# Optimization experiments

Hardware: AMD Instinct MI355X
Metric: run time of the kernel (lower is better)

## Reference

```python
import jax, jax.numpy as jnp
import numpy as np

B, T, H = 8, 8192, 512
E, R = 4, 16
SCALE = 0.04  # ~1/sqrt(H), keeps activations/logits in a sane range


def setup_inputs() -> dict:
    key = jax.random.key(0)
    ks = jax.random.split(key, 7)
    return {
        "x": jax.random.normal(ks[0], (B, T, H), jnp.float32),
        "gate_w": jax.random.normal(ks[1], (E, H), jnp.float32) * SCALE,
        "thr_w": jax.random.normal(ks[2], (1, H), jnp.float32) * SCALE,
        "fc1_w": jax.random.normal(ks[3], (E, H, H), jnp.float32) * SCALE,
        "lora_A": jax.random.normal(ks[4], (E, H, R), jnp.float32) * SCALE,
        "lora_B": jax.random.normal(ks[5], (E, R, H), jnp.float32) * SCALE,
        "fc2_w": jax.random.normal(ks[6], (E, H, H), jnp.float32) * SCALE,
    }


def reference(x, gate_w, thr_w, fc1_w, lora_A, lora_B, fc2_w):
    b, t, h = x.shape
    e = gate_w.shape[0]
    xf = x.reshape(-1, h)  # [N, H], N = B*T

    # Threshold-gated routing
    gate_logits = jax.nn.softmax(xf @ gate_w.T, axis=-1)          # [N, E]
    thresholds = jax.nn.sigmoid(xf @ thr_w.T) * (1.0 / e)         # [N, 1]
    adapted = gate_logits - thresholds                            # [N, E]
    selected = (adapted >= 0).astype(xf.dtype)                    # [N, E]
    weights = adapted * selected
    wsum = jnp.sum(weights, axis=-1, keepdims=True)
    wsum = jnp.where(wsum == 0, jnp.ones_like(wsum), wsum)
    weights = weights / wsum                                      # [N, E]

    # Experts: fc2(relu(fc1(x)) @ A @ B). Dense over all experts; the
    # weighted combine with zero weights matches the gather/scatter path.
    hidden = jax.nn.relu(jnp.einsum('ni,ehi->neh', xf, fc1_w))    # [N, E, H]
    lo = jnp.einsum('neh,ehr->ner', hidden, lora_A)               # [N, E, R]
    lo = jnp.einsum('ner,ero->neo', lo, lora_B)                   # [N, E, H]
    expert_out = jnp.einsum('neo,edo->ned', lo, fc2_w)            # [N, E, H]

    out = jnp.einsum('ne,ned->nd', weights, expert_out)           # [N, H]
    return out.reshape(b, t, h)
```

## Files before the change

### kernel.cpp

```cpp
#include <hip/hip_runtime.h>
#include <stdint.h>

#define NTOK 65536
#define HD   512
#define EXP  4
#define RK   16

typedef __attribute__((ext_vector_type(8)))  short short8;
typedef __attribute__((ext_vector_type(4)))  float f32x4;
typedef __attribute__((ext_vector_type(16))) float f32x16;

__device__ __forceinline__ unsigned short f2bf(float f) {
  union { float f; unsigned int u; } c; c.f = f;
  return (unsigned short)((c.u + 0x7fffu + ((c.u >> 16) & 1u)) >> 16);
}

__device__ __forceinline__ void gl_lds16(const void* g, void* l) {
  __builtin_amdgcn_global_load_lds((const __attribute__((address_space(1))) void*)g,
                                   (__attribute__((address_space(3))) void*)l, 16, 0, 0);
}

__global__ void convgate(const float* __restrict__ x, const float* __restrict__ gw,
                         const float* __restrict__ tw, unsigned short* __restrict__ xbo,
                         float* __restrict__ gates) {
  const int tid = threadIdx.x;
  const int wave = tid >> 6, lane = tid & 63;
  const int half = lane >> 5, l32 = lane & 31;
  const int base = blockIdx.x * 32 + wave * 8;

  float4 wv[5][4];
#pragma unroll
  for (int e = 0; e < 4; e++) {
    const float4* wr = (const float4*)(gw + e * HD);
#pragma unroll
    for (int j = 0; j < 4; j++) wv[e][j] = wr[l32 * 4 + j];
  }
  {
    const float4* wr = (const float4*)tw;
#pragma unroll
    for (int j = 0; j < 4; j++) wv[4][j] = wr[l32 * 4 + j];
  }

#pragma unroll
  for (int it = 0; it < 4; it++) {
    const int n = base + it * 2 + half;
    const float4* xr = (const float4*)(x + (size_t)n * HD);
    float4 xv[4];
#pragma unroll
    for (int j = 0; j < 4; j++) xv[j] = xr[l32 * 4 + j];

    union { short8 v; unsigned short s[8]; } pa, pb;
    pa.s[0] = f2bf(xv[0].x); pa.s[1] = f2bf(xv[0].y); pa.s[2] = f2bf(xv[0].z); pa.s[3] = f2bf(xv[0].w);
    pa.s[4] = f2bf(xv[1].x); pa.s[5] = f2bf(xv[1].y); pa.s[6] = f2bf(xv[1].z); pa.s[7] = f2bf(xv[1].w);
    pb.s[0] = f2bf(xv[2].x); pb.s[1] = f2bf(xv[2].y); pb.s[2] = f2bf(xv[2].z); pb.s[3] = f2bf(xv[2].w);
    pb.s[4] = f2bf(xv[3].x); pb.s[5] = f2bf(xv[3].y); pb.s[6] = f2bf(xv[3].z); pb.s[7] = f2bf(xv[3].w);
    short8* xo = (short8*)(xbo + (size_t)n * HD + l32 * 16);
    xo[0] = pa.v; xo[1] = pb.v;

    float s[5];
#pragma unroll
    for (int e = 0; e < 5; e++) {
      s[e] = 0.f;
#pragma unroll
      for (int j = 0; j < 4; j++)
        s[e] += xv[j].x * wv[e][j].x + xv[j].y * wv[e][j].y
              + xv[j].z * wv[e][j].z + xv[j].w * wv[e][j].w;
    }
#pragma unroll
    for (int off = 16; off > 0; off >>= 1)
#pragma unroll
      for (int i = 0; i < 5; i++) s[i] += __shfl_xor(s[i], off, 64);

    float m = fmaxf(fmaxf(s[0], s[1]), fmaxf(s[2], s[3]));
    float e0 = expf(s[0] - m), e1 = expf(s[1] - m), e2 = expf(s[2] - m), e3 = expf(s[3] - m);
    float inv = 1.f / (e0 + e1 + e2 + e3);
    float thr = 0.25f / (1.f + expf(-s[4]));
    float a0 = e0 * inv - thr, a1 = e1 * inv - thr, a2 = e2 * inv - thr, a3 = e3 * inv - thr;
    float w0 = a0 > 0.f ? a0 : 0.f, w1 = a1 > 0.f ? a1 : 0.f;
    float w2 = a2 > 0.f ? a2 : 0.f, w3 = a3 > 0.f ? a3 : 0.f;
    float wsum = w0 + w1 + w2 + w3;
    wsum = (wsum == 0.f) ? 1.f : wsum;
    if (l32 < 4) {
      float wval = l32 == 0 ? w0 : l32 == 1 ? w1 : l32 == 2 ? w2 : w3;
      gates[(size_t)n * 4 + l32] = wval / wsum;
    }
  }
}

__global__ void prep_all(const float* __restrict__ fc1w, unsigned short* __restrict__ w1b,
                         const float* __restrict__ la, unsigned short* __restrict__ laT,
                         const float* __restrict__ loraB, const float* __restrict__ fc2,
                         unsigned short* __restrict__ Mt) {
  const int bid = blockIdx.x, tid = threadIdx.x;
  if (bid < 1024) {
    int i = bid * 256 + tid;
    float4 v = ((const float4*)fc1w)[i];
    ushort4 u;
    u.x = f2bf(v.x); u.y = f2bf(v.y); u.z = f2bf(v.z); u.w = f2bf(v.w);
    ((ushort4*)w1b)[i] = u;
  } else if (bid < 1152) {
    int idx = (bid - 1024) * 256 + tid;
    int h = idx & (HD - 1);
    int er = idx >> 9;
    int e = er >> 4, r = er & 15;
    laT[(size_t)er * HD + h] = f2bf(la[((size_t)e * HD + h) * RK + r]);
  } else {
    const int wid = (bid - 1152) * 4 + (tid >> 6);
    const int lane = tid & 63;
    const int d = wid & (HD - 1);
    const int er = wid >> 9;
    const int e = er >> 4, r = er & 15;
    const float4* B = (const float4*)(loraB + ((size_t)e * RK + r) * HD);
    const float4* F = (const float4*)(fc2 + ((size_t)e * HD + d) * HD);
    const float4 b0 = B[lane * 2], b1 = B[lane * 2 + 1];
    const float4 f0 = F[lane * 2], f1 = F[lane * 2 + 1];
    float s = b0.x * f0.x + b0.y * f0.y + b0.z * f0.z + b0.w * f0.w
            + b1.x * f1.x + b1.y * f1.y + b1.z * f1.z + b1.w * f1.w;
#pragma unroll
    for (int off = 32; off > 0; off >>= 1) s += __shfl_xor(s, off, 64);
    if (lane == 0) Mt[d * 64 + er] = f2bf(s);
  }
}

__launch_bounds__(512, 2)
__global__ void fc1_lora(const unsigned short* __restrict__ xb,
                         const unsigned short* __restrict__ w1b,
                         const unsigned short* __restrict__ laT,
                         float* __restrict__ lw) {
  __shared__ __align__(16) char smem[135168];
  const int bid = blockIdx.x;
  const int c = bid & 7;
  const int j = bid >> 3;
  const int eh = j & 7;
  const int e = eh >> 1, hq = eh & 1;
  const int ntile = c * 32 + (j >> 3);
  const int n0 = ntile * 256;
  const int tid = threadIdx.x;
  const int wave = tid >> 6, lane = tid & 63;
  const int l16 = lane & 15, quad = lane >> 4;
  const int l32 = lane & 31, half = lane >> 5;
  const int wr = wave >> 2, wc = wave & 3;

  const unsigned short* xg = xb + (size_t)n0 * HD;
  const unsigned short* wg = w1b + ((size_t)e * HD + (size_t)hq * 256) * HD;

  const unsigned short* xsrc[2];
  const unsigned short* wsrc[2];
#pragma unroll
  for (int i = 0; i < 2; i++) {
    const int sl = tid + 512 * i;
    const int sr = sl >> 3, g8 = (sl & 7) ^ (sr & 7);
    const int row = sr * 2 + (g8 >> 2), g = g8 & 3;
    xsrc[i] = xg + (size_t)row * HD + g * 8;
    wsrc[i] = wg + (size_t)row * HD + g * 8;
  }
  const int wbase = wave * 1024;

  int axo[2][4], bxo[2][2];
#pragma unroll
  for (int p = 0; p < 2; p++) {
#pragma unroll
    for (int mb = 0; mb < 4; mb++) {
      const int rowa = wr * 128 + mb * 32 + l32;
      const int sr = rowa >> 1, g8 = (rowa & 1) * 4 + p * 2 + half;
      axo[p][mb] = (sr * 8 + (g8 ^ (sr & 7))) * 16;
    }
#pragma unroll
    for (int nb = 0; nb < 2; nb++) {
      const int rowb = wc * 64 + nb * 32 + l32;
      const int sr = rowb >> 1, g8 = (rowb & 1) * 4 + p * 2 + half;
      bxo[p][nb] = (sr * 8 + (g8 ^ (sr & 7))) * 16;
    }
  }

  f32x16 acc[4][2];
#pragma unroll
  for (int mb = 0; mb < 4; mb++)
#pragma unroll
    for (int nb = 0; nb < 2; nb++)
#pragma unroll
      for (int r = 0; r < 16; r++) acc[mb][nb][r] = 0.f;

#pragma unroll
  for (int tt = 0; tt < 3; tt++) {
    char* As = smem + tt * 32768;
#pragma unroll
    for (int i = 0; i < 2; i++) gl_lds16(xsrc[i] + tt * 32, As + wbase + 8192 * i);
#pragma unroll
    for (int i = 0; i < 2; i++) gl_lds16(wsrc[i] + tt * 32, As + 16384 + wbase + 8192 * i);
  }
  asm volatile("s_waitcnt vmcnt(8)" ::: "memory");
  __builtin_amdgcn_s_barrier();
  __builtin_amdgcn_sched_barrier(0);

#pragma unroll
  for (int t = 0; t < 16; t++) {
    char* Ab = smem + (t & 3) * 32768;
    char* Bb = Ab + 16384;
    char* As = smem + ((t + 3) & 3) * 32768;
    const int kos = (t + 3) * 32;
#pragma unroll
    for (int p = 0; p < 2; p++) {
      short8 af[4], bf[2];
#pragma unroll
      for (int mb = 0; mb < 4; mb++) af[mb] = *(const short8*)(Ab + axo[p][mb]);
#pragma unroll
      for (int nb = 0; nb < 2; nb++) bf[nb] = *(const short8*)(Bb + bxo[p][nb]);
      if (t < 13) {
        gl_lds16(xsrc[p] + kos, As + wbase + 8192 * p);
        gl_lds16(wsrc[p] + kos, As + 16384 + wbase + 8192 * p);
      }
      __builtin_amdgcn_s_barrier();
      asm volatile("s_waitcnt lgkmcnt(0)" ::: "memory");
      __builtin_amdgcn_sched_barrier(0);
      __builtin_amdgcn_s_setprio(1);
#pragma unroll
      for (int mb = 0; mb < 4; mb++)
#pragma unroll
        for (int nb = 0; nb < 2; nb++)
          acc[mb][nb] = __builtin_amdgcn_mfma_f32_32x32x16_bf16(af[mb], bf[nb], acc[mb][nb], 0, 0, 0);
      __builtin_amdgcn_s_setprio(0);
      if (p == 0) {
        __builtin_amdgcn_s_barrier();
      } else {
        if (t < 13)       asm volatile("s_waitcnt vmcnt(8)" ::: "memory");
        else if (t == 13) asm volatile("s_waitcnt vmcnt(4)" ::: "memory");
        else if (t == 14) asm volatile("s_waitcnt vmcnt(0)" ::: "memory");
        __builtin_amdgcn_s_barrier();
      }
      __builtin_amdgcn_sched_barrier(0);
    }
  }

  unsigned short* hsm = (unsigned short*)smem;
#pragma unroll
  for (int mb = 0; mb < 4; mb++)
#pragma unroll
    for (int nb = 0; nb < 2; nb++) {
      const int colh = wc * 64 + nb * 32 + l32;
#pragma unroll
      for (int r = 0; r < 16; r++) {
        const int tok = wr * 128 + mb * 32 + 4 * half + (r & 3) + 8 * (r >> 2);
        float v = acc[mb][nb][r];
        v = v > 0.f ? v : 0.f;
        hsm[tok * 264 + colh] = f2bf(v);
      }
    }
  __syncthreads();

  const unsigned short* laTe = laT + (size_t)(e * 16 + l16) * HD + hq * 256;
  f32x4 lo[2];
#pragma unroll
  for (int mf = 0; mf < 2; mf++)
#pragma unroll
    for (int i = 0; i < 4; i++) lo[mf][i] = 0.f;
#pragma unroll
  for (int k2 = 0; k2 < 8; k2++) {
    const short8 b2 = *(const short8*)(laTe + k2 * 32 + quad * 8);
#pragma unroll
    for (int mf = 0; mf < 2; mf++) {
      const int tok = wave * 32 + mf * 16 + l16;
      const short8 a2 = *(const short8*)(hsm + tok * 264 + k2 * 32 + quad * 8);
      lo[mf] = __builtin_amdgcn_mfma_f32_16x16x32_bf16(a2, b2, lo[mf], 0, 0, 0);
    }
  }
#pragma unroll
  for (int mf = 0; mf < 2; mf++)
#pragma unroll
    for (int i = 0; i < 4; i++)
      atomicAdd(lw + (size_t)(n0 + wave * 32 + mf * 16 + quad * 4 + i) * 64 + e * 16 + l16, lo[mf][i]);
}

__launch_bounds__(256, 2)
__global__ void combine_k(const float* __restrict__ lw, const float* __restrict__ gates,
                          const unsigned short* __restrict__ Mt, float* __restrict__ out) {
  __shared__ __align__(16) char smem[65536];
  const int n0 = blockIdx.x * 64;
  const int tid = threadIdx.x;
  const int wave = tid >> 6, lane = tid & 63, quad = lane >> 4, l16 = lane & 15;
#pragma unroll
  for (int i = 0; i < 16; i++) {
    const int slot = tid + 256 * i;
    const int row = slot >> 3;
    const int g = (slot & 7) ^ (row & 7);
    *(uint4*)(smem + slot * 16) = *(const uint4*)(Mt + row * 64 + g * 8);
  }
  __syncthreads();
  f32x4 acc[4][8];
#pragma unroll
  for (int a = 0; a < 4; a++)
#pragma unroll
    for (int b = 0; b < 8; b++)
#pragma unroll
      for (int i = 0; i < 4; i++) acc[a][b][i] = 0.f;
#pragma unroll
  for (int ks = 0; ks < 2; ks++) {
    short8 af[4], bfr[8];
#pragma unroll
    for (int mf = 0; mf < 4; mf++) {
      const int n = n0 + mf * 16 + l16;
      const float* lr = lw + (size_t)n * 64 + ks * 32 + quad * 8;
      float4 u0 = *(const float4*)lr;
      float4 u1 = *(const float4*)(lr + 4);
      const float g = gates[(size_t)n * 4 + ((ks * 32 + quad * 8) >> 4)];
      union { short8 v; unsigned short s[8]; } a;
      a.s[0] = f2bf(u0.x * g); a.s[1] = f2bf(u0.y * g);
      a.s[2] = f2bf(u0.z * g); a.s[3] = f2bf(u0.w * g);
      a.s[4] = f2bf(u1.x * g); a.s[5] = f2bf(u1.y * g);
      a.s[6] = f2bf(u1.z * g); a.s[7] = f2bf(u1.w * g);
      af[mf] = a.v;
    }
#pragma unroll
    for (int nf = 0; nf < 8; nf++) {
      const int row = wave * 128 + nf * 16 + l16;
      const int slot = row * 8 + ((ks * 4 + quad) ^ (row & 7));
      bfr[nf] = *(const short8*)(smem + slot * 16);
    }
#pragma unroll
    for (int mf = 0; mf < 4; mf++)
#pragma unroll
      for (int nf = 0; nf < 8; nf++)
        acc[mf][nf] = __builtin_amdgcn_mfma_f32_16x16x32_bf16(af[mf], bfr[nf], acc[mf][nf], 0, 0, 0);
  }
  __syncthreads();
  float* scr = (float*)smem + wave * 320;
#pragma unroll
  for (int mf = 0; mf < 4; mf++)
#pragma unroll
    for (int nf = 0; nf < 8; nf++) {
#pragma unroll
      for (int i = 0; i < 4; i++) scr[(quad * 4 + i) * 20 + l16] = acc[mf][nf][i];
      float4 v = *(const float4*)(scr + l16 * 20 + quad * 4);
      *(float4*)(out + (size_t)(n0 + mf * 16 + l16) * HD + wave * 128 + nf * 16 + quad * 4) = v;
    }
}

extern "C" void kernel_launch(void* const* d_in, const int* in_sizes, int n_in,
                              void* d_out, int out_size, void* d_ws, size_t ws_size,
                              hipStream_t stream) {
  const float* x      = (const float*)d_in[0];
  const float* gate_w = (const float*)d_in[1];
  const float* thr_w  = (const float*)d_in[2];
  const float* fc1_w  = (const float*)d_in[3];
  const float* lora_A = (const float*)d_in[4];
  const float* lora_B = (const float*)d_in[5];
  const float* fc2_w  = (const float*)d_in[6];
  float* out = (float*)d_out;
  char* ws = (char*)d_ws;

  unsigned short* xbp = (unsigned short*)(ws);
  unsigned short* w1b = (unsigned short*)(ws + 67108864);
  unsigned short* Mt  = (unsigned short*)(ws + 69206016);
  float*          gts = (float*)(ws + 69271552);
  float*          lwp = (float*)(ws + 70320128);
  unsigned short* laT = (unsigned short*)(ws + 87097344);

  hipMemsetAsync(lwp, 0, (size_t)NTOK * 64 * sizeof(float), stream);
  convgate<<<NTOK / 32, 256, 0, stream>>>(x, gate_w, thr_w, xbp, gts);
  prep_all<<<9344, 256, 0, stream>>>(fc1_w, w1b, lora_A, laT, lora_B, fc2_w, Mt);
  fc1_lora<<<2048, 512, 0, stream>>>(xbp, w1b, laT, lwp);
  combine_k<<<NTOK / 64, 256, 0, stream>>>(lwp, gts, Mt, out);
}
```

Measured before the change: 438.8 us.

## Fuse x bf16 conversion and gate routing into fc1 GEMM, drop atomics

Removes the separate convgate kernel. fc1_lora now loads fp32 x directly through registers, converts it to bf16 into LDS, and computes the gate and threshold logits with an extra MFMA against a packed gate-weight tile, only in the eh==0 blocks. The pipeline drops from a 4-stage to a 3-stage LDS ring, with A staged through registers and B loaded asynchronously. The atomicAdd into a memset buffer becomes plain stores into two per-half buffers that combine_k sums, which also removes the memset. In exchange, the x reads are repeated across the 8 expert/half blocks per token tile, in fp32 instead of bf16, which doubles that read traffic. The shallower prefetch may also expose more latency.

```diff
diff --git a/kernel.cpp b/kernel.cpp
--- a/kernel.cpp
+++ b/kernel.cpp
@@ -20,77 +20,12 @@
                                    (__attribute__((address_space(3))) void*)l, 16, 0, 0);
 }
 
-__global__ void convgate(const float* __restrict__ x, const float* __restrict__ gw,
-                         const float* __restrict__ tw, unsigned short* __restrict__ xbo,
-                         float* __restrict__ gates) {
-  const int tid = threadIdx.x;
-  const int wave = tid >> 6, lane = tid & 63;
-  const int half = lane >> 5, l32 = lane & 31;
-  const int base = blockIdx.x * 32 + wave * 8;
-
-  float4 wv[5][4];
-#pragma unroll
-  for (int e = 0; e < 4; e++) {
-    const float4* wr = (const float4*)(gw + e * HD);
-#pragma unroll
-    for (int j = 0; j < 4; j++) wv[e][j] = wr[l32 * 4 + j];
-  }
-  {
-    const float4* wr = (const float4*)tw;
-#pragma unroll
-    for (int j = 0; j < 4; j++) wv[4][j] = wr[l32 * 4 + j];
-  }
-
-#pragma unroll
-  for (int it = 0; it < 4; it++) {
-    const int n = base + it * 2 + half;
-    const float4* xr = (const float4*)(x + (size_t)n * HD);
-    float4 xv[4];
-#pragma unroll
-    for (int j = 0; j < 4; j++) xv[j] = xr[l32 * 4 + j];
-
-    union { short8 v; unsigned short s[8]; } pa, pb;
-    pa.s[0] = f2bf(xv[0].x); pa.s[1] = f2bf(xv[0].y); pa.s[2] = f2bf(xv[0].z); pa.s[3] = f2bf(xv[0].w);
-    pa.s[4] = f2bf(xv[1].x); pa.s[5] = f2bf(xv[1].y); pa.s[6] = f2bf(xv[1].z); pa.s[7] = f2bf(xv[1].w);
-    pb.s[0] = f2bf(xv[2].x); pb.s[1] = f2bf(xv[2].y); pb.s[2] = f2bf(xv[2].z); pb.s[3] = f2bf(xv[2].w);
-    pb.s[4] = f2bf(xv[3].x); pb.s[5] = f2bf(xv[3].y); pb.s[6] = f2bf(xv[3].z); pb.s[7] = f2bf(xv[3].w);
-    short8* xo = (short8*)(xbo + (size_t)n * HD + l32 * 16);
-    xo[0] = pa.v; xo[1] = pb.v;
-
-    float s[5];
-#pragma unroll
-    for (int e = 0; e < 5; e++) {
-      s[e] = 0.f;
-#pragma unroll
-      for (int j = 0; j < 4; j++)
-        s[e] += xv[j].x * wv[e][j].x + xv[j].y * wv[e][j].y
-              + xv[j].z * wv[e][j].z + xv[j].w * wv[e][j].w;
-    }
-#pragma unroll
-    for (int off = 16; off > 0; off >>= 1)
-#pragma unroll
-      for (int i = 0; i < 5; i++) s[i] += __shfl_xor(s[i], off, 64);
-
-    float m = fmaxf(fmaxf(s[0], s[1]), fmaxf(s[2], s[3]));
-    float e0 = expf(s[0] - m), e1 = expf(s[1] - m), e2 = expf(s[2] - m), e3 = expf(s[3] - m);
-    float inv = 1.f / (e0 + e1 + e2 + e3);
-    float thr = 0.25f / (1.f + expf(-s[4]));
-    float a0 = e0 * inv - thr, a1 = e1 * inv - thr, a2 = e2 * inv - thr, a3 = e3 * inv - thr;
-    float w0 = a0 > 0.f ? a0 : 0.f, w1 = a1 > 0.f ? a1 : 0.f;
-    float w2 = a2 > 0.f ? a2 : 0.f, w3 = a3 > 0.f ? a3 : 0.f;
-    float wsum = w0 + w1 + w2 + w3;
-    wsum = (wsum == 0.f) ? 1.f : wsum;
-    if (l32 < 4) {
-      float wval = l32 == 0 ? w0 : l32 == 1 ? w1 : l32 == 2 ? w2 : w3;
-      gates[(size_t)n * 4 + l32] = wval / wsum;
-    }
-  }
-}
-
 __global__ void prep_all(const float* __restrict__ fc1w, unsigned short* __restrict__ w1b,
                          const float* __restrict__ la, unsigned short* __restrict__ laT,
                          const float* __restrict__ loraB, const float* __restrict__ fc2,
-                         unsigned short* __restrict__ Mt) {
+                         unsigned short* __restrict__ Mt,
+                         const float* __restrict__ gw, const float* __restrict__ tw,
+                         unsigned short* __restrict__ gwp) {
   const int bid = blockIdx.x, tid = threadIdx.x;
   if (bid < 1024) {
     int i = bid * 256 + tid;
@@ -104,7 +39,7 @@
     int er = idx >> 9;
     int e = er >> 4, r = er & 15;
     laT[(size_t)er * HD + h] = f2bf(la[((size_t)e * HD + h) * RK + r]);
-  } else {
+  } else if (bid < 9344) {
     const int wid = (bid - 1152) * 4 + (tid >> 6);
     const int lane = tid & 63;
     const int d = wid & (HD - 1);
@@ -119,14 +54,30 @@
 #pragma unroll
     for (int off = 32; off > 0; off >>= 1) s += __shfl_xor(s, off, 64);
     if (lane == 0) Mt[d * 64 + er] = f2bf(s);
+  } else {
+    const int pair = (bid - 9344) * 256 + tid;
+    const int s = pair >> 6, ln = pair & 63;
+    const int col = ln & 31;
+    const int kb = s * 16 + (ln >> 5) * 8;
+    union { short8 v; unsigned short u[8]; } o;
+#pragma unroll
+    for (int jj = 0; jj < 8; jj++) {
+      float v = 0.f;
+      if (col < 4) v = gw[col * HD + kb + jj];
+      else if (col == 4) v = tw[kb + jj];
+      o.u[jj] = f2bf(v);
+    }
+    *(short8*)(gwp + (size_t)pair * 8) = o.v;
   }
 }
 
 __launch_bounds__(512, 2)
-__global__ void fc1_lora(const unsigned short* __restrict__ xb,
+__global__ void fc1_lora(const float* __restrict__ x,
                          const unsigned short* __restrict__ w1b,
                          const unsigned short* __restrict__ laT,
-                         float* __restrict__ lw) {
+                         const unsigned short* __restrict__ gwp,
+                         float* __restrict__ lw,
+                         float* __restrict__ gates) {
   __shared__ __align__(16) char smem[135168];
   const int bid = blockIdx.x;
   const int c = bid & 7;
@@ -140,23 +91,23 @@
   const int l16 = lane & 15, quad = lane >> 4;
   const int l32 = lane & 31, half = lane >> 5;
   const int wr = wave >> 2, wc = wave & 3;
-
-  const unsigned short* xg = xb + (size_t)n0 * HD;
+  const bool gateB = (eh == 0);
+
   const unsigned short* wg = w1b + ((size_t)e * HD + (size_t)hq * 256) * HD;
 
-  const unsigned short* xsrc[2];
+  const float4* asrc[2];
   const unsigned short* wsrc[2];
 #pragma unroll
   for (int i = 0; i < 2; i++) {
     const int sl = tid + 512 * i;
     const int sr = sl >> 3, g8 = (sl & 7) ^ (sr & 7);
     const int row = sr * 2 + (g8 >> 2), g = g8 & 3;
-    xsrc[i] = xg + (size_t)row * HD + g * 8;
+    asrc[i] = (const float4*)(x + (size_t)(n0 + row) * HD + g * 8);
     wsrc[i] = wg + (size_t)row * HD + g * 8;
   }
   const int wbase = wave * 1024;
 
-  int axo[2][4], bxo[2][2];
+  int axo[2][4], bxo[2][2], axg[2];
 #pragma unroll
   for (int p = 0; p < 2; p++) {
 #pragma unroll
@@ -171,6 +122,9 @@
       const int sr = rowb >> 1, g8 = (rowb & 1) * 4 + p * 2 + half;
       bxo[p][nb] = (sr * 8 + (g8 ^ (sr & 7))) * 16;
     }
+    const int rowg = wave * 32 + l32;
+    const int srg = rowg >> 1, g8g = (rowg & 1) * 4 + p * 2 + half;
+    axg[p] = (srg * 8 + (g8g ^ (srg & 7))) * 16;
   }
 
   f32x16 acc[4][2];
@@ -180,35 +134,63 @@
     for (int nb = 0; nb < 2; nb++)
 #pragma unroll
       for (int r = 0; r < 16; r++) acc[mb][nb][r] = 0.f;
-
-#pragma unroll
-  for (int tt = 0; tt < 3; tt++) {
-    char* As = smem + tt * 32768;
-#pragma unroll
-    for (int i = 0; i < 2; i++) gl_lds16(xsrc[i] + tt * 32, As + wbase + 8192 * i);
-#pragma unroll
-    for (int i = 0; i < 2; i++) gl_lds16(wsrc[i] + tt * 32, As + 16384 + wbase + 8192 * i);
-  }
-  asm volatile("s_waitcnt vmcnt(8)" ::: "memory");
+  f32x16 gacc;
+#pragma unroll
+  for (int r = 0; r < 16; r++) gacc[r] = 0.f;
+
+  char* gwl = smem + 98304;
+  float4 abuf[4];
+
+  if (gateB) {
+#pragma unroll
+    for (int i = 0; i < 4; i++)
+      gl_lds16((const char*)gwp + tid * 16 + i * 8192, gwl + wbase + i * 8192);
+  }
+  abuf[0] = asrc[0][0]; abuf[1] = asrc[0][1];
+  abuf[2] = asrc[1][0]; abuf[3] = asrc[1][1];
+#pragma unroll
+  for (int i = 0; i < 2; i++) gl_lds16(wsrc[i], smem + 16384 + wbase + 8192 * i);
+#pragma unroll
+  for (int i = 0; i < 2; i++) gl_lds16(wsrc[i] + 32, smem + 32768 + 16384 + wbase + 8192 * i);
+  asm volatile("s_waitcnt vmcnt(2)" ::: "memory");
+  {
+    union { short8 v; unsigned short u[8]; } wa, wb;
+    wa.u[0] = f2bf(abuf[0].x); wa.u[1] = f2bf(abuf[0].y); wa.u[2] = f2bf(abuf[0].z); wa.u[3] = f2bf(abuf[0].w);
+    wa.u[4] = f2bf(abuf[1].x); wa.u[5] = f2bf(abuf[1].y); wa.u[6] = f2bf(abuf[1].z); wa.u[7] = f2bf(abuf[1].w);
+    wb.u[0] = f2bf(abuf[2].x); wb.u[1] = f2bf(abuf[2].y); wb.u[2] = f2bf(abuf[2].z); wb.u[3] = f2bf(abuf[2].w);
+    wb.u[4] = f2bf(abuf[3].x); wb.u[5] = f2bf(abuf[3].y); wb.u[6] = f2bf(abuf[3].z); wb.u[7] = f2bf(abuf[3].w);
+    *(short8*)(smem + tid * 16) = wa.v;
+    *(short8*)(smem + tid * 16 + 8192) = wb.v;
+  }
+  asm volatile("s_waitcnt lgkmcnt(0)" ::: "memory");
   __builtin_amdgcn_s_barrier();
   __builtin_amdgcn_sched_barrier(0);
 
 #pragma unroll
   for (int t = 0; t < 16; t++) {
-    char* Ab = smem + (t & 3) * 32768;
+    char* Ab = smem + (t % 3) * 32768;
     char* Bb = Ab + 16384;
-    char* As = smem + ((t + 3) & 3) * 32768;
-    const int kos = (t + 3) * 32;
 #pragma unroll
     for (int p = 0; p < 2; p++) {
-      short8 af[4], bf[2];
+      short8 af[4], bf[2], gaf, gwb;
 #pragma unroll
       for (int mb = 0; mb < 4; mb++) af[mb] = *(const short8*)(Ab + axo[p][mb]);
 #pragma unroll
       for (int nb = 0; nb < 2; nb++) bf[nb] = *(const short8*)(Bb + bxo[p][nb]);
-      if (t < 13) {
-        gl_lds16(xsrc[p] + kos, As + wbase + 8192 * p);
-        gl_lds16(wsrc[p] + kos, As + 16384 + wbase + 8192 * p);
+      if (gateB) {
+        gaf = *(const short8*)(Ab + axg[p]);
+        gwb = *(const short8*)(gwl + (t * 2 + p) * 1024 + lane * 16);
+      }
+      if (p == 0 && t < 15) {
+        const int a4 = (t + 1) * 8;
+        abuf[0] = asrc[0][a4]; abuf[1] = asrc[0][a4 + 1];
+        abuf[2] = asrc[1][a4]; abuf[3] = asrc[1][a4 + 1];
+      }
+      if (p == 1 && t < 14) {
+        const int kos = (t + 2) * 32;
+        char* Bs = smem + ((t + 2) % 3) * 32768 + 16384;
+        gl_lds16(wsrc[0] + kos, Bs + wbase);
+        gl_lds16(wsrc[1] + kos, Bs + wbase + 8192);
       }
       __builtin_amdgcn_s_barrier();
       asm volatile("s_waitcnt lgkmcnt(0)" ::: "memory");
@@ -219,17 +201,58 @@
 #pragma unroll
         for (int nb = 0; nb < 2; nb++)
           acc[mb][nb] = __builtin_amdgcn_mfma_f32_32x32x16_bf16(af[mb], bf[nb], acc[mb][nb], 0, 0, 0);
+      if (gateB)
+        gacc = __builtin_amdgcn_mfma_f32_32x32x16_bf16(gaf, gwb, gacc, 0, 0, 0);
       __builtin_amdgcn_s_setprio(0);
       if (p == 0) {
         __builtin_amdgcn_s_barrier();
       } else {
-        if (t < 13)       asm volatile("s_waitcnt vmcnt(8)" ::: "memory");
-        else if (t == 13) asm volatile("s_waitcnt vmcnt(4)" ::: "memory");
+        if (t < 14)       asm volatile("s_waitcnt vmcnt(2)" ::: "memory");
         else if (t == 14) asm volatile("s_waitcnt vmcnt(0)" ::: "memory");
+        if (t < 15) {
+          char* Aw = smem + ((t + 1) % 3) * 32768;
+          union { short8 v; unsigned short u[8]; } wa, wb2;
+          wa.u[0] = f2bf(abuf[0].x); wa.u[1] = f2bf(abuf[0].y); wa.u[2] = f2bf(abuf[0].z); wa.u[3] = f2bf(abuf[0].w);
+          wa.u[4] = f2bf(abuf[1].x); wa.u[5] = f2bf(abuf[1].y); wa.u[6] = f2bf(abuf[1].z); wa.u[7] = f2bf(abuf[1].w);
+          wb2.u[0] = f2bf(abuf[2].x); wb2.u[1] = f2bf(abuf[2].y); wb2.u[2] = f2bf(abuf[2].z); wb2.u[3] = f2bf(abuf[2].w);
+          wb2.u[4] = f2bf(abuf[3].x); wb2.u[5] = f2bf(abuf[3].y); wb2.u[6] = f2bf(abuf[3].z); wb2.u[7] = f2bf(abuf[3].w);
+          *(short8*)(Aw + tid * 16) = wa.v;
+          *(short8*)(Aw + tid * 16 + 8192) = wb2.v;
+        }
+        asm volatile("s_waitcnt lgkmcnt(0)" ::: "memory");
         __builtin_amdgcn_s_barrier();
       }
       __builtin_amdgcn_sched_barrier(0);
     }
+  }
+
+  if (gateB) {
+    float* gsm = (float*)smem;
+    if (l32 < 5) {
+#pragma unroll
+      for (int r = 0; r < 16; r++) {
+        const int row32 = 4 * half + (r & 3) + 8 * (r >> 2);
+        gsm[(wave * 32 + row32) * 8 + l32] = gacc[r];
+      }
+    }
+    __syncthreads();
+    if (tid < 256) {
+      const float s0 = gsm[tid * 8 + 0], s1 = gsm[tid * 8 + 1];
+      const float s2 = gsm[tid * 8 + 2], s3 = gsm[tid * 8 + 3];
+      const float s4 = gsm[tid * 8 + 4];
+      float m = fmaxf(fmaxf(s0, s1), fmaxf(s2, s3));
+      float e0 = expf(s0 - m), e1 = expf(s1 - m), e2 = expf(s2 - m), e3 = expf(s3 - m);
+      float inv = 1.f / (e0 + e1 + e2 + e3);
+      float thr = 0.25f / (1.f + expf(-s4));
+      float a0 = e0 * inv - thr, a1 = e1 * inv - thr, a2 = e2 * inv - thr, a3 = e3 * inv - thr;
+      float w0 = a0 > 0.f ? a0 : 0.f, w1 = a1 > 0.f ? a1 : 0.f;
+      float w2 = a2 > 0.f ? a2 : 0.f, w3 = a3 > 0.f ? a3 : 0.f;
+      float wsum = w0 + w1 + w2 + w3;
+      wsum = (wsum == 0.f) ? 1.f : wsum;
+      float4 gv; gv.x = w0 / wsum; gv.y = w1 / wsum; gv.z = w2 / wsum; gv.w = w3 / wsum;
+      *(float4*)(gates + (size_t)(n0 + tid) * 4) = gv;
+    }
+    __syncthreads();
   }
 
   unsigned short* hsm = (unsigned short*)smem;
@@ -264,11 +287,12 @@
       lo[mf] = __builtin_amdgcn_mfma_f32_16x16x32_bf16(a2, b2, lo[mf], 0, 0, 0);
     }
   }
+  float* lwh = lw + (size_t)hq * NTOK * 64;
 #pragma unroll
   for (int mf = 0; mf < 2; mf++)
 #pragma unroll
     for (int i = 0; i < 4; i++)
-      atomicAdd(lw + (size_t)(n0 + wave * 32 + mf * 16 + quad * 4 + i) * 64 + e * 16 + l16, lo[mf][i]);
+      lwh[(size_t)(n0 + wave * 32 + mf * 16 + quad * 4 + i) * 64 + e * 16 + l16] = lo[mf][i];
 }
 
 __launch_bounds__(256, 2)
@@ -299,9 +323,13 @@
 #pragma unroll
     for (int mf = 0; mf < 4; mf++) {
       const int n = n0 + mf * 16 + l16;
-      const float* lr = lw + (size_t)n * 64 + ks * 32 + quad * 8;
-      float4 u0 = *(const float4*)lr;
-      float4 u1 = *(const float4*)(lr + 4);
+      const float* lr0 = lw + (size_t)n * 64 + ks * 32 + quad * 8;
+      const float* lr1 = lr0 + (size_t)NTOK * 64;
+      float4 a0 = *(const float4*)lr0,       a1 = *(const float4*)(lr0 + 4);
+      float4 b0 = *(const float4*)lr1,       b1 = *(const float4*)(lr1 + 4);
+      float4 u0, u1;
+      u0.x = a0.x + b0.x; u0.y = a0.y + b0.y; u0.z = a0.z + b0.z; u0.w = a0.w + b0.w;
+      u1.x = a1.x + b1.x; u1.y = a1.y + b1.y; u1.z = a1.z + b1.z; u1.w = a1.w + b1.w;
       const float g = gates[(size_t)n * 4 + ((ks * 32 + quad * 8) >> 4)];
       union { short8 v; unsigned short s[8]; } a;
       a.s[0] = f2bf(u0.x * g); a.s[1] = f2bf(u0.y * g);
@@ -348,16 +376,15 @@
   float* out = (float*)d_out;
   char* ws = (char*)d_ws;
 
-  unsigned short* xbp = (unsigned short*)(ws);
-  unsigned short* w1b = (unsigned short*)(ws + 67108864);
-  unsigned short* Mt  = (unsigned short*)(ws + 69206016);
-  float*          gts = (float*)(ws + 69271552);
-  float*          lwp = (float*)(ws + 70320128);
-  unsigned short* laT = (unsigned short*)(ws + 87097344);
-
-  hipMemsetAsync(lwp, 0, (size_t)NTOK * 64 * sizeof(float), stream);
-  convgate<<<NTOK / 32, 256, 0, stream>>>(x, gate_w, thr_w, xbp, gts);
-  prep_all<<<9344, 256, 0, stream>>>(fc1_w, w1b, lora_A, laT, lora_B, fc2_w, Mt);
-  fc1_lora<<<2048, 512, 0, stream>>>(xbp, w1b, laT, lwp);
+  float*          lwp = (float*)(ws);
+  unsigned short* w1b = (unsigned short*)(ws + 33554432);
+  unsigned short* Mt  = (unsigned short*)(ws + 35651584);
+  unsigned short* laT = (unsigned short*)(ws + 35717120);
+  unsigned short* gwp = (unsigned short*)(ws + 35782656);
+  float*          gts = (float*)(ws + 35815424);
+
+  prep_all<<<9352, 256, 0, stream>>>(fc1_w, w1b, lora_A, laT, lora_B, fc2_w, Mt,
+                                     gate_w, thr_w, gwp);
+  fc1_lora<<<2048, 512, 0, stream>>>(x, w1b, laT, gwp, lwp, gts);
   combine_k<<<NTOK / 64, 256, 0, stream>>>(lwp, gts, Mt, out);
 }
```

New measurement: 440.7 us. About the same (+0.4%).
